# Kernel tuning notes

Hardware: AMD Instinct MI355X
Metric: run time of the kernel (lower is better)

Reference implementation:

```python
import jax, jax.numpy as jnp
import numpy as np

B, T, H, L2 = 131072, 4, 8, 5  # T=4 forced by conv1 in_channels=4; L2 = layers 1..5 of the 6-layer lstm1


def _lstm_dir(xs, w_ih, w_hh, b, h0, c0):
    # xs: [T, B, Din] -> hs: [T, B, H]; PyTorch gate order i, f, g, o
    def step(carry, xt):
        h, c = carry
        g = xt @ w_ih.T + h @ w_hh.T + b
        i, f, gg, o = jnp.split(g, 4, axis=-1)
        c = jax.nn.sigmoid(f) * c + jax.nn.sigmoid(i) * jnp.tanh(gg)
        h = jax.nn.sigmoid(o) * jnp.tanh(c)
        return (h, c), h
    _, hs = jax.lax.scan(step, (h0, c0), xs)
    return hs


def _bilstm(xs, wi_f, wh_f, b_f, wi_b, wh_b, b_b, h0f, c0f, h0b, c0b):
    hf = _lstm_dir(xs, wi_f, wh_f, b_f, h0f, c0f)
    hb = _lstm_dir(xs[::-1], wi_b, wh_b, b_b, h0b, c0b)[::-1]
    return jnp.concatenate([hf, hb], axis=-1)  # [T, B, 2H]


def _conv1d(x, w, b):
    # x: [B, C, L], w: [O, I, K] (torch Conv1d layout)
    y = jax.lax.conv_general_dilated(x, w, (1,), [(0, 0)], dimension_numbers=('NCH', 'OIH', 'NCH'))
    return y + b[None, :, None]


def _deconv1d(x, w, b):
    # torch ConvTranspose1d weight [I, O, K]; stride 1, pad 0 == full conv with flipped kernel
    k = w.shape[-1]
    wk = jnp.flip(jnp.swapaxes(w, 0, 1), -1)  # [O, I, K]
    y = jax.lax.conv_general_dilated(x, wk, (1,), [(k - 1, k - 1)], dimension_numbers=('NCH', 'OIH', 'NCH'))
    return y + b[None, :, None]


def setup_inputs():
    key = jax.random.key(0)
    ks = iter(jax.random.split(key, 32))
    rn = lambda shape, s=0.2: jax.random.normal(next(ks), shape, jnp.float32) * s
    return {
        'x': rn((B, T, 2), 1.0),
        'h0': rn((12, B, H), 1.0),
        'c0': rn((12, B, H), 1.0),
        'w_ih0': rn((2, 4 * H, 2)),
        'w_hh0': rn((2, 4 * H, H)),
        'b_ih0': rn((2, 4 * H)),
        'b_hh0': rn((2, 4 * H)),
        'w_ih': rn((L2, 2, 4 * H, 2 * H)),
        'w_hh': rn((L2, 2, 4 * H, H)),
        'b_ih': rn((L2, 2, 4 * H)),
        'b_hh': rn((L2, 2, 4 * H)),
        'conv1_w': rn((8, 4, 2)), 'conv1_b': rn((8,)),
        'conv2_w': rn((16, 8, 2)), 'conv2_b': rn((16,)),
        'deconv1_w': rn((16, 8, 2)), 'deconv1_b': rn((8,)),
        'deconv2_w': rn((8, 4, 2)), 'deconv2_b': rn((4,)),
        'fc1_w': rn((8, 16)), 'fc1_b': rn((8,)),
        'fc2_w': rn((4, 8)), 'fc2_b': rn((4,)),
    }


def reference(x, h0, c0, w_ih0, w_hh0, b_ih0, b_hh0, w_ih, w_hh, b_ih, b_hh,
              conv1_w, conv1_b, conv2_w, conv2_b, deconv1_w, deconv1_b,
              deconv2_w, deconv2_b, fc1_w, fc1_b, fc2_w, fc2_b):
    xs = jnp.swapaxes(x, 0, 1)  # [T, B, 2]
    y = _bilstm(xs, w_ih0[0], w_hh0[0], b_ih0[0] + b_hh0[0],
                w_ih0[1], w_hh0[1], b_ih0[1] + b_hh0[1],
                h0[0], c0[0], h0[1], c0[1])
    for l in range(L2):  # fixed, small layer count (eval mode: inter-layer dropout off)
        i = 2 * (l + 1)
        y = _bilstm(y, w_ih[l, 0], w_hh[l, 0], b_ih[l, 0] + b_hh[l, 0],
                    w_ih[l, 1], w_hh[l, 1], b_ih[l, 1] + b_hh[l, 1],
                    h0[i], c0[i], h0[i + 1], c0[i + 1])
    y = jax.nn.sigmoid(jnp.swapaxes(y, 0, 1))  # [B, 4, 16]; dim 1 acts as conv channels
    y = _conv1d(y, conv1_w, conv1_b)           # [B, 8, 15]
    y = _conv1d(y, conv2_w, conv2_b)           # [B, 16, 14]
    y = _deconv1d(y, deconv1_w, deconv1_b)     # [B, 8, 15]
    y = _deconv1d(y, deconv2_w, deconv2_b)     # [B, 4, 16]
    y = y @ fc1_w.T + fc1_b                    # [B, 4, 8]
    y = y @ fc2_w.T + fc2_b                    # [B, 4, 4]
    return jnp.tanh(y)
```

## Files before the change

kernel.cpp:

```cpp
#include <hip/hip_runtime.h>
#include <hip/hip_bf16.h>


using f32x2 = __attribute__((ext_vector_type(2))) float;
using f32x4 = __attribute__((ext_vector_type(4))) float;

#define OFF_WIH0 0
#define OFF_WHH0 128
#define OFF_B0   640
#define OFF_WIH  704
#define OFF_WHH  5824
#define OFF_B    8384
#define OFF_M    9024
#define OFF_MB   10048

__device__ __forceinline__ float rcpf_(float x) {
#if __has_builtin(__builtin_amdgcn_rcpf)
    return __builtin_amdgcn_rcpf(x);
#else
    return 1.0f / x;
#endif
}
__device__ __forceinline__ float exp2f_(float x) {
#if __has_builtin(__builtin_amdgcn_exp2f)
    return __builtin_amdgcn_exp2f(x);
#else
    return exp2f(x);
#endif
}
__device__ __forceinline__ float sigm(float x) {
    return rcpf_(1.0f + exp2f_(-1.44269504f * x));
}
__device__ __forceinline__ float tanhx(float x) {
    return fmaf(2.0f, rcpf_(1.0f + exp2f_(-2.88539008f * x)), -1.0f);
}

__global__ __launch_bounds__(256) void prep_all(
    const float* __restrict__ wih0, const float* __restrict__ whh0,
    const float* __restrict__ bih0, const float* __restrict__ bhh0,
    const float* __restrict__ wih,  const float* __restrict__ whh,
    const float* __restrict__ bih,  const float* __restrict__ bhh,
    const float* __restrict__ c1w, const float* __restrict__ c1b,
    const float* __restrict__ c2w, const float* __restrict__ c2b,
    const float* __restrict__ d1w, const float* __restrict__ d1b,
    const float* __restrict__ d2w, const float* __restrict__ d2b,
    const float* __restrict__ f1w, const float* __restrict__ f1b,
    const float* __restrict__ f2w, const float* __restrict__ f2b,
    float* __restrict__ W)
{
    __shared__ float A[13][232];
    __shared__ float Bf[13][232];
    const int tid = threadIdx.x;

    if (blockIdx.x < 36) {
        int t = blockIdx.x * 256 + tid;
        const int n = 36 * 256;
        for (int i = t; i < 128; i += n)  W[OFF_WIH0 + i] = wih0[i];
        for (int i = t; i < 512; i += n)  W[OFF_WHH0 + i] = whh0[i];
        for (int i = t; i < 64; i += n)   W[OFF_B0 + i] = bih0[i] + bhh0[i];
        for (int i = t; i < 5120; i += n) W[OFF_WIH + i] = wih[i];
        for (int i = t; i < 2560; i += n) W[OFF_WHH + i] = whh[i];
        for (int i = t; i < 640; i += n)  W[OFF_B + i] = bih[i] + bhh[i];
        return;
    }
    const int base = (blockIdx.x - 36) * 13;

    for (int idx = tid; idx < 13 * 64; idx += 256) {
        int cl = idx / 64, r = idx % 64;
        A[cl][r] = (base + cl == r) ? 1.0f : 0.0f;
    }
    __syncthreads();
    for (int idx = tid; idx < 13 * 120; idx += 256) {
        int cl = idx / 120, rr = idx % 120; int o = rr / 15, l = rr % 15;
        float acc = (base + cl == 64) ? c1b[o] : 0.0f;
        for (int i = 0; i < 4; i++)
            for (int kk = 0; kk < 2; kk++)
                acc += c1w[(o * 4 + i) * 2 + kk] * A[cl][i * 16 + l + kk];
        Bf[cl][rr] = acc;
    }
    __syncthreads();
    for (int idx = tid; idx < 13 * 224; idx += 256) {
        int cl = idx / 224, rr = idx % 224; int o = rr / 14, l = rr % 14;
        float acc = (base + cl == 64) ? c2b[o] : 0.0f;
        for (int i = 0; i < 8; i++)
            for (int kk = 0; kk < 2; kk++)
                acc += c2w[(o * 8 + i) * 2 + kk] * Bf[cl][i * 15 + l + kk];
        A[cl][rr] = acc;
    }
    __syncthreads();
    for (int idx = tid; idx < 13 * 120; idx += 256) {
        int cl = idx / 120, rr = idx % 120; int o = rr / 15, l = rr % 15;
        float acc = (base + cl == 64) ? d1b[o] : 0.0f;
        for (int i = 0; i < 16; i++)
            for (int kk = 0; kk < 2; kk++) {
                int ls = l - kk;
                if (ls >= 0 && ls < 14)
                    acc += d1w[(i * 8 + o) * 2 + kk] * A[cl][i * 14 + ls];
            }
        Bf[cl][rr] = acc;
    }
    __syncthreads();
    for (int idx = tid; idx < 13 * 64; idx += 256) {
        int cl = idx / 64, rr = idx % 64; int o = rr / 16, l = rr % 16;
        float acc = (base + cl == 64) ? d2b[o] : 0.0f;
        for (int i = 0; i < 8; i++)
            for (int kk = 0; kk < 2; kk++) {
                int ls = l - kk;
                if (ls >= 0 && ls < 15)
                    acc += d2w[(i * 4 + o) * 2 + kk] * Bf[cl][i * 15 + ls];
            }
        A[cl][rr] = acc;
    }
    __syncthreads();
    for (int idx = tid; idx < 13 * 32; idx += 256) {
        int cl = idx / 32, rr = idx % 32; int ch = rr / 8, jj = rr % 8;
        float acc = (base + cl == 64) ? f1b[jj] : 0.0f;
        for (int l = 0; l < 16; l++)
            acc += f1w[jj * 16 + l] * A[cl][ch * 16 + l];
        Bf[cl][rr] = acc;
    }
    __syncthreads();
    for (int idx = tid; idx < 13 * 16; idx += 256) {
        int cl = idx / 16, rr = idx % 16; int ch = rr / 4, m = rr % 4;
        int col = base + cl;
        if (col > 64) continue;
        float acc = (col == 64) ? f2b[m] : 0.0f;
        for (int j = 0; j < 8; j++)
            acc += f2w[m * 8 + j] * Bf[cl][ch * 8 + j];
        if (col < 64) W[OFF_M + rr * 64 + col] = acc;
        else          W[OFF_MB + rr] = acc;
    }
}

template<bool FWD, bool LAST>
__device__ __forceinline__ void layer16(
    const float* __restrict__ Wi, const float* __restrict__ Wh,
    const float* __restrict__ Bs,
    const float* __restrict__ h0s, const float* __restrict__ c0s,
    int gelem0, int u,
    float* const (&lin)[2], float* const (&lout)[2])
{
    f32x4 wiv[4][4];
    f32x4 whv[4][2];
    f32x4 bsv;
#pragma unroll
    for (int g = 0; g < 4; g++) {
        const int r = u + 8 * g;
        const f32x4* wr = reinterpret_cast<const f32x4*>(Wi + r * 16);
        wiv[g][0] = wr[0]; wiv[g][1] = wr[1]; wiv[g][2] = wr[2]; wiv[g][3] = wr[3];
        const f32x4* ur = reinterpret_cast<const f32x4*>(Wh + r * 8);
        whv[g][0] = ur[0]; whv[g][1] = ur[1];
        bsv[g] = Bs[r];
    }
    f32x4 hg[2][2];
    float cc[2];
#pragma unroll
    for (int e = 0; e < 2; e++) {
        const f32x4* hp = reinterpret_cast<const f32x4*>(h0s + (size_t)(gelem0 + e) * 8);
        hg[e][0] = hp[0]; hg[e][1] = hp[1];
        cc[e] = c0s[(size_t)(gelem0 + e) * 8 + u];
    }
    float hreg[2][4];
    const int off = FWD ? 0 : 8;

#pragma unroll
    for (int s = 0; s < 4; s++) {
        const int t = FWD ? s : 3 - s;
        const int tprev = FWD ? t - 1 : t + 1;
        f32x2 acc[2][4];
#pragma unroll
        for (int e = 0; e < 2; e++) {
            const f32x4* ip = reinterpret_cast<const f32x4*>(lin[e] + 16 * t);
            f32x4 i0 = ip[0], i1 = ip[1], i2 = ip[2], i3 = ip[3];
            f32x4 ha, hb;
            if (s == 0) { ha = hg[e][0]; hb = hg[e][1]; }
            else {
                const f32x4* hp = reinterpret_cast<const f32x4*>(lout[e] + 16 * tprev + off);
                ha = hp[0]; hb = hp[1];
            }
            f32x2 xin[8];
            xin[0] = f32x2{i0.x, i0.y}; xin[1] = f32x2{i0.z, i0.w};
            xin[2] = f32x2{i1.x, i1.y}; xin[3] = f32x2{i1.z, i1.w};
            xin[4] = f32x2{i2.x, i2.y}; xin[5] = f32x2{i2.z, i2.w};
            xin[6] = f32x2{i3.x, i3.y}; xin[7] = f32x2{i3.z, i3.w};
            f32x2 hx[4];
            hx[0] = f32x2{ha.x, ha.y}; hx[1] = f32x2{ha.z, ha.w};
            hx[2] = f32x2{hb.x, hb.y}; hx[3] = f32x2{hb.z, hb.w};
#pragma unroll
            for (int g = 0; g < 4; g++) {
                f32x2 a = f32x2{bsv[g], 0.0f};
#pragma unroll
                for (int j = 0; j < 4; j++) {
                    f32x2 wlo = f32x2{wiv[g][j].x, wiv[g][j].y};
                    f32x2 whi = f32x2{wiv[g][j].z, wiv[g][j].w};
                    a = __builtin_elementwise_fma(xin[2 * j], wlo, a);
                    a = __builtin_elementwise_fma(xin[2 * j + 1], whi, a);
                }
#pragma unroll
                for (int j = 0; j < 2; j++) {
                    f32x2 wlo = f32x2{whv[g][j].x, whv[g][j].y};
                    f32x2 whi = f32x2{whv[g][j].z, whv[g][j].w};
                    a = __builtin_elementwise_fma(hx[2 * j], wlo, a);
                    a = __builtin_elementwise_fma(hx[2 * j + 1], whi, a);
                }
                acc[e][g] = a;
            }
        }
#pragma unroll
        for (int e = 0; e < 2; e++) {
            float si = sigm(acc[e][0].x + acc[e][0].y);
            float sf = sigm(acc[e][1].x + acc[e][1].y);
            float tg = tanhx(acc[e][2].x + acc[e][2].y);
            float so = sigm(acc[e][3].x + acc[e][3].y);
            cc[e] = fmaf(sf, cc[e], si * tg);
            float hn = so * tanhx(cc[e]);
            lout[e][16 * t + off + u] = hn;
            if (LAST) hreg[e][s] = hn;
        }
    }
    if (LAST) {
#pragma unroll
        for (int e = 0; e < 2; e++)
#pragma unroll
            for (int s = 0; s < 4; s++) {
                const int t = FWD ? s : 3 - s;
                lout[e][16 * t + off + u] = sigm(hreg[e][s]);
            }
    }
}

template<bool FWD>
__device__ __forceinline__ void layer2(
    const float* __restrict__ Wi, const float* __restrict__ Wh,
    const float* __restrict__ Bs,
    const float* __restrict__ h0s, const float* __restrict__ c0s,
    int gelem0, int u,
    const f32x2 (&xin2)[2][4], float* const (&lout)[2])
{
    f32x2 wiv[4];
    f32x4 whv[4][2];
    f32x4 bsv;
#pragma unroll
    for (int g = 0; g < 4; g++) {
        const int r = u + 8 * g;
        wiv[g] = *reinterpret_cast<const f32x2*>(Wi + r * 2);
        const f32x4* ur = reinterpret_cast<const f32x4*>(Wh + r * 8);
        whv[g][0] = ur[0]; whv[g][1] = ur[1];
        bsv[g] = Bs[r];
    }
    f32x4 hg[2][2];
    float cc[2];
#pragma unroll
    for (int e = 0; e < 2; e++) {
        const f32x4* hp = reinterpret_cast<const f32x4*>(h0s + (size_t)(gelem0 + e) * 8);
        hg[e][0] = hp[0]; hg[e][1] = hp[1];
        cc[e] = c0s[(size_t)(gelem0 + e) * 8 + u];
    }
    const int off = FWD ? 0 : 8;

#pragma unroll
    for (int s = 0; s < 4; s++) {
        const int t = FWD ? s : 3 - s;
        const int tprev = FWD ? t - 1 : t + 1;
        f32x2 acc[2][4];
#pragma unroll
        for (int e = 0; e < 2; e++) {
            f32x4 ha, hb;
            if (s == 0) { ha = hg[e][0]; hb = hg[e][1]; }
            else {
                const f32x4* hp = reinterpret_cast<const f32x4*>(lout[e] + 16 * tprev + off);
                ha = hp[0]; hb = hp[1];
            }
            f32x2 hx[4];
            hx[0] = f32x2{ha.x, ha.y}; hx[1] = f32x2{ha.z, ha.w};
            hx[2] = f32x2{hb.x, hb.y}; hx[3] = f32x2{hb.z, hb.w};
#pragma unroll
            for (int g = 0; g < 4; g++) {
                f32x2 a = __builtin_elementwise_fma(xin2[e][t], wiv[g], f32x2{bsv[g], 0.0f});
#pragma unroll
                for (int j = 0; j < 2; j++) {
                    f32x2 wlo = f32x2{whv[g][j].x, whv[g][j].y};
                    f32x2 whi = f32x2{whv[g][j].z, whv[g][j].w};
                    a = __builtin_elementwise_fma(hx[2 * j], wlo, a);
                    a = __builtin_elementwise_fma(hx[2 * j + 1], whi, a);
                }
                acc[e][g] = a;
            }
        }
#pragma unroll
        for (int e = 0; e < 2; e++) {
            float si = sigm(acc[e][0].x + acc[e][0].y);
            float sf = sigm(acc[e][1].x + acc[e][1].y);
            float tg = tanhx(acc[e][2].x + acc[e][2].y);
            float so = sigm(acc[e][3].x + acc[e][3].y);
            cc[e] = fmaf(sf, cc[e], si * tg);
            lout[e][16 * t + off + u] = so * tanhx(cc[e]);
        }
    }
}

__global__ __launch_bounds__(256, 3) void lstm_main(
    const float* __restrict__ x, const float* __restrict__ h0,
    const float* __restrict__ c0, const float* __restrict__ W,
    float* __restrict__ out, int B)
{
    __shared__ float yb[2][64 * 68];
    const int tid = threadIdx.x;
    const int u = tid & 7;
    const int slot = tid >> 3;
    const int row0 = slot * 2;
    const int gelem0 = blockIdx.x * 64 + row0;

    float* y0[2]; float* y1[2];
#pragma unroll
    for (int e = 0; e < 2; e++) {
        y0[e] = &yb[0][(row0 + e) * 68];
        y1[e] = &yb[1][(row0 + e) * 68];
    }

    f32x2 xin2[2][4];
#pragma unroll
    for (int e = 0; e < 2; e++) {
        const f32x4* xp = reinterpret_cast<const f32x4*>(x + (size_t)(gelem0 + e) * 8);
        f32x4 a = xp[0], b = xp[1];
        xin2[e][0] = f32x2{a.x, a.y}; xin2[e][1] = f32x2{a.z, a.w};
        xin2[e][2] = f32x2{b.x, b.y}; xin2[e][3] = f32x2{b.z, b.w};
    }

    layer2<true>(W + OFF_WIH0, W + OFF_WHH0, W + OFF_B0,
                 h0 + (size_t)0 * B * 8, c0 + (size_t)0 * B * 8,
                 gelem0, u, xin2, y0);
    layer2<false>(W + OFF_WIH0 + 64, W + OFF_WHH0 + 256, W + OFF_B0 + 32,
                  h0 + (size_t)1 * B * 8, c0 + (size_t)1 * B * 8,
                  gelem0, u, xin2, y0);

#pragma unroll
    for (int l = 1; l <= 4; l++) {
        float* const (&lin)[2] = (l & 1) ? y0 : y1;
        float* const (&lout)[2] = (l & 1) ? y1 : y0;
        const float* wi = W + OFF_WIH + (size_t)(l - 1) * 1024;
        const float* wh = W + OFF_WHH + (size_t)(l - 1) * 512;
        const float* bb = W + OFF_B + (size_t)(l - 1) * 64;
        const int si = 2 * l;
        layer16<true, false>(wi, wh, bb,
                             h0 + (size_t)si * B * 8, c0 + (size_t)si * B * 8,
                             gelem0, u, lin, lout);
        layer16<false, false>(wi + 512, wh + 256, bb + 32,
                              h0 + (size_t)(si + 1) * B * 8, c0 + (size_t)(si + 1) * B * 8,
                              gelem0, u, lin, lout);
    }
    {
        const float* wi = W + OFF_WIH + (size_t)4 * 1024;
        const float* wh = W + OFF_WHH + (size_t)4 * 512;
        const float* bb = W + OFF_B + (size_t)4 * 64;
        layer16<true, true>(wi, wh, bb,
                            h0 + (size_t)10 * B * 8, c0 + (size_t)10 * B * 8,
                            gelem0, u, y0, y1);
        layer16<false, true>(wi + 512, wh + 256, bb + 32,
                             h0 + (size_t)11 * B * 8, c0 + (size_t)11 * B * 8,
                             gelem0, u, y0, y1);
    }

    {
        const int o0 = 2 * u, o1 = 2 * u + 1;
        const f32x4* M0 = reinterpret_cast<const f32x4*>(W + OFF_M + o0 * 64);
        const f32x4* M1 = reinterpret_cast<const f32x4*>(W + OFF_M + o1 * 64);
        const float b0 = W[OFF_MB + o0];
        const float b1 = W[OFF_MB + o1];
#pragma unroll
        for (int e = 0; e < 2; e++) {
            float a0 = b0, a1 = b1;
#pragma unroll
            for (int q = 0; q < 16; q++) {
                f32x4 sv = *reinterpret_cast<const f32x4*>(y1[e] + 4 * q);
                f32x4 m0 = M0[q], m1 = M1[q];
                a0 = fmaf(sv.x, m0.x, a0); a0 = fmaf(sv.y, m0.y, a0);
                a0 = fmaf(sv.z, m0.z, a0); a0 = fmaf(sv.w, m0.w, a0);
                a1 = fmaf(sv.x, m1.x, a1); a1 = fmaf(sv.y, m1.y, a1);
                a1 = fmaf(sv.z, m1.z, a1); a1 = fmaf(sv.w, m1.w, a1);
            }
            f32x2 res;
            res.x = tanhx(a0);
            res.y = tanhx(a1);
            *reinterpret_cast<f32x2*>(out + (size_t)(gelem0 + e) * 16 + 2 * u) = res;
        }
    }
}

extern "C" void kernel_launch(void* const* d_in, const int* in_sizes, int n_in,
                              void* d_out, int out_size, void* d_ws, size_t ws_size,
                              hipStream_t stream)
{
    const float* x    = (const float*)d_in[0];
    const float* h0   = (const float*)d_in[1];
    const float* c0   = (const float*)d_in[2];
    const float* wih0 = (const float*)d_in[3];
    const float* whh0 = (const float*)d_in[4];
    const float* bih0 = (const float*)d_in[5];
    const float* bhh0 = (const float*)d_in[6];
    const float* wih  = (const float*)d_in[7];
    const float* whh  = (const float*)d_in[8];
    const float* bih  = (const float*)d_in[9];
    const float* bhh  = (const float*)d_in[10];
    const float* c1w  = (const float*)d_in[11];
    const float* c1b  = (const float*)d_in[12];
    const float* c2w  = (const float*)d_in[13];
    const float* c2b  = (const float*)d_in[14];
    const float* d1w  = (const float*)d_in[15];
    const float* d1b  = (const float*)d_in[16];
    const float* d2w  = (const float*)d_in[17];
    const float* d2b  = (const float*)d_in[18];
    const float* f1w  = (const float*)d_in[19];
    const float* f1b  = (const float*)d_in[20];
    const float* f2w  = (const float*)d_in[21];
    const float* f2b  = (const float*)d_in[22];

    float* W = (float*)d_ws;
    const int B = in_sizes[0] / 8;

    prep_all<<<41, 256, 0, stream>>>(wih0, whh0, bih0, bhh0, wih, whh, bih, bhh,
                                     c1w, c1b, c2w, c2b, d1w, d1b, d2w, d2b,
                                     f1w, f1b, f2w, f2b, W);
    lstm_main<<<B / 64, 256, 0, stream>>>(x, h0, c0, W, (float*)d_out, B);
}
```

Measured before the change: 350.3 us.

## Hoist input projections out of LSTM recurrence and raise occupancy bound

Each LSTM layer now computes the input-to-hidden projections for all four timesteps up front, before the sequential recurrence, so the serial loop only does the small hidden-state matvec plus activations. This shortens the dependent chain per step and lets the input loads and FMAs run without waiting on the previous step. It needs 32 extra live floats per thread for the precomputed gates, while the launch bound minimum blocks per CU goes from 3 to 4, which tightens the register budget and may cause spills.

```diff
diff --git a/kernel.cpp b/kernel.cpp
--- a/kernel.cpp
+++ b/kernel.cpp
@@ -141,51 +141,26 @@
     float* const (&lin)[2], float* const (&lout)[2])
 {
     f32x4 wiv[4][4];
-    f32x4 whv[4][2];
     f32x4 bsv;
 #pragma unroll
     for (int g = 0; g < 4; g++) {
         const int r = u + 8 * g;
         const f32x4* wr = reinterpret_cast<const f32x4*>(Wi + r * 16);
         wiv[g][0] = wr[0]; wiv[g][1] = wr[1]; wiv[g][2] = wr[2]; wiv[g][3] = wr[3];
-        const f32x4* ur = reinterpret_cast<const f32x4*>(Wh + r * 8);
-        whv[g][0] = ur[0]; whv[g][1] = ur[1];
         bsv[g] = Bs[r];
     }
-    f32x4 hg[2][2];
-    float cc[2];
+    float z[2][4][4];
 #pragma unroll
     for (int e = 0; e < 2; e++) {
-        const f32x4* hp = reinterpret_cast<const f32x4*>(h0s + (size_t)(gelem0 + e) * 8);
-        hg[e][0] = hp[0]; hg[e][1] = hp[1];
-        cc[e] = c0s[(size_t)(gelem0 + e) * 8 + u];
-    }
-    float hreg[2][4];
-    const int off = FWD ? 0 : 8;
-
-#pragma unroll
-    for (int s = 0; s < 4; s++) {
-        const int t = FWD ? s : 3 - s;
-        const int tprev = FWD ? t - 1 : t + 1;
-        f32x2 acc[2][4];
-#pragma unroll
-        for (int e = 0; e < 2; e++) {
+#pragma unroll
+        for (int t = 0; t < 4; t++) {
             const f32x4* ip = reinterpret_cast<const f32x4*>(lin[e] + 16 * t);
             f32x4 i0 = ip[0], i1 = ip[1], i2 = ip[2], i3 = ip[3];
-            f32x4 ha, hb;
-            if (s == 0) { ha = hg[e][0]; hb = hg[e][1]; }
-            else {
-                const f32x4* hp = reinterpret_cast<const f32x4*>(lout[e] + 16 * tprev + off);
-                ha = hp[0]; hb = hp[1];
-            }
             f32x2 xin[8];
             xin[0] = f32x2{i0.x, i0.y}; xin[1] = f32x2{i0.z, i0.w};
             xin[2] = f32x2{i1.x, i1.y}; xin[3] = f32x2{i1.z, i1.w};
             xin[4] = f32x2{i2.x, i2.y}; xin[5] = f32x2{i2.z, i2.w};
             xin[6] = f32x2{i3.x, i3.y}; xin[7] = f32x2{i3.z, i3.w};
-            f32x2 hx[4];
-            hx[0] = f32x2{ha.x, ha.y}; hx[1] = f32x2{ha.z, ha.w};
-            hx[2] = f32x2{hb.x, hb.y}; hx[3] = f32x2{hb.z, hb.w};
 #pragma unroll
             for (int g = 0; g < 4; g++) {
                 f32x2 a = f32x2{bsv[g], 0.0f};
@@ -196,22 +171,61 @@
                     a = __builtin_elementwise_fma(xin[2 * j], wlo, a);
                     a = __builtin_elementwise_fma(xin[2 * j + 1], whi, a);
                 }
-#pragma unroll
-                for (int j = 0; j < 2; j++) {
-                    f32x2 wlo = f32x2{whv[g][j].x, whv[g][j].y};
-                    f32x2 whi = f32x2{whv[g][j].z, whv[g][j].w};
-                    a = __builtin_elementwise_fma(hx[2 * j], wlo, a);
-                    a = __builtin_elementwise_fma(hx[2 * j + 1], whi, a);
-                }
-                acc[e][g] = a;
+                z[e][t][g] = a.x + a.y;
             }
         }
+    }
+
+    f32x4 whv[4][2];
+#pragma unroll
+    for (int g = 0; g < 4; g++) {
+        const f32x4* ur = reinterpret_cast<const f32x4*>(Wh + (u + 8 * g) * 8);
+        whv[g][0] = ur[0]; whv[g][1] = ur[1];
+    }
+    f32x4 hg[2][2];
+    float cc[2];
+#pragma unroll
+    for (int e = 0; e < 2; e++) {
+        const f32x4* hp = reinterpret_cast<const f32x4*>(h0s + (size_t)(gelem0 + e) * 8);
+        hg[e][0] = hp[0]; hg[e][1] = hp[1];
+        cc[e] = c0s[(size_t)(gelem0 + e) * 8 + u];
+    }
+    float hreg[2][4];
+    const int off = FWD ? 0 : 8;
+
+#pragma unroll
+    for (int s = 0; s < 4; s++) {
+        const int t = FWD ? s : 3 - s;
+        const int tprev = FWD ? t - 1 : t + 1;
 #pragma unroll
         for (int e = 0; e < 2; e++) {
-            float si = sigm(acc[e][0].x + acc[e][0].y);
-            float sf = sigm(acc[e][1].x + acc[e][1].y);
-            float tg = tanhx(acc[e][2].x + acc[e][2].y);
-            float so = sigm(acc[e][3].x + acc[e][3].y);
+            f32x4 ha, hb;
+            if (s == 0) { ha = hg[e][0]; hb = hg[e][1]; }
+            else {
+                const f32x4* hp = reinterpret_cast<const f32x4*>(lout[e] + 16 * tprev + off);
+                ha = hp[0]; hb = hp[1];
+            }
+            f32x2 hx[4];
+            hx[0] = f32x2{ha.x, ha.y}; hx[1] = f32x2{ha.z, ha.w};
+            hx[2] = f32x2{hb.x, hb.y}; hx[3] = f32x2{hb.z, hb.w};
+            float gate[4];
+#pragma unroll
+            for (int g = 0; g < 4; g++) {
+                f32x2 a = f32x2{z[e][t][g], 0.0f};
+                f32x2 wlo0 = f32x2{whv[g][0].x, whv[g][0].y};
+                f32x2 whi0 = f32x2{whv[g][0].z, whv[g][0].w};
+                f32x2 wlo1 = f32x2{whv[g][1].x, whv[g][1].y};
+                f32x2 whi1 = f32x2{whv[g][1].z, whv[g][1].w};
+                a = __builtin_elementwise_fma(hx[0], wlo0, a);
+                a = __builtin_elementwise_fma(hx[1], whi0, a);
+                a = __builtin_elementwise_fma(hx[2], wlo1, a);
+                a = __builtin_elementwise_fma(hx[3], whi1, a);
+                gate[g] = a.x + a.y;
+            }
+            float si = sigm(gate[0]);
+            float sf = sigm(gate[1]);
+            float tg = tanhx(gate[2]);
+            float so = sigm(gate[3]);
             cc[e] = fmaf(sf, cc[e], si * tg);
             float hn = so * tanhx(cc[e]);
             lout[e][16 * t + off + u] = hn;
@@ -238,15 +252,28 @@
     const f32x2 (&xin2)[2][4], float* const (&lout)[2])
 {
     f32x2 wiv[4];
-    f32x4 whv[4][2];
     f32x4 bsv;
 #pragma unroll
     for (int g = 0; g < 4; g++) {
         const int r = u + 8 * g;
         wiv[g] = *reinterpret_cast<const f32x2*>(Wi + r * 2);
-        const f32x4* ur = reinterpret_cast<const f32x4*>(Wh + r * 8);
+        bsv[g] = Bs[r];
+    }
+    float z[2][4][4];
+#pragma unroll
+    for (int e = 0; e < 2; e++)
+#pragma unroll
+        for (int t = 0; t < 4; t++)
+#pragma unroll
+            for (int g = 0; g < 4; g++)
+                z[e][t][g] = fmaf(xin2[e][t].x, wiv[g].x,
+                             fmaf(xin2[e][t].y, wiv[g].y, bsv[g]));
+
+    f32x4 whv[4][2];
+#pragma unroll
+    for (int g = 0; g < 4; g++) {
+        const f32x4* ur = reinterpret_cast<const f32x4*>(Wh + (u + 8 * g) * 8);
         whv[g][0] = ur[0]; whv[g][1] = ur[1];
-        bsv[g] = Bs[r];
     }
     f32x4 hg[2][2];
     float cc[2];
@@ -262,7 +289,6 @@
     for (int s = 0; s < 4; s++) {
         const int t = FWD ? s : 3 - s;
         const int tprev = FWD ? t - 1 : t + 1;
-        f32x2 acc[2][4];
 #pragma unroll
         for (int e = 0; e < 2; e++) {
             f32x4 ha, hb;
@@ -274,32 +300,31 @@
             f32x2 hx[4];
             hx[0] = f32x2{ha.x, ha.y}; hx[1] = f32x2{ha.z, ha.w};
             hx[2] = f32x2{hb.x, hb.y}; hx[3] = f32x2{hb.z, hb.w};
+            float gate[4];
 #pragma unroll
             for (int g = 0; g < 4; g++) {
-                f32x2 a = __builtin_elementwise_fma(xin2[e][t], wiv[g], f32x2{bsv[g], 0.0f});
-#pragma unroll
-                for (int j = 0; j < 2; j++) {
-                    f32x2 wlo = f32x2{whv[g][j].x, whv[g][j].y};
-                    f32x2 whi = f32x2{whv[g][j].z, whv[g][j].w};
-                    a = __builtin_elementwise_fma(hx[2 * j], wlo, a);
-                    a = __builtin_elementwise_fma(hx[2 * j + 1], whi, a);
-                }
-                acc[e][g] = a;
-            }
-        }
-#pragma unroll
-        for (int e = 0; e < 2; e++) {
-            float si = sigm(acc[e][0].x + acc[e][0].y);
-            float sf = sigm(acc[e][1].x + acc[e][1].y);
-            float tg = tanhx(acc[e][2].x + acc[e][2].y);
-            float so = sigm(acc[e][3].x + acc[e][3].y);
+                f32x2 a = f32x2{z[e][t][g], 0.0f};
+                f32x2 wlo0 = f32x2{whv[g][0].x, whv[g][0].y};
+                f32x2 whi0 = f32x2{whv[g][0].z, whv[g][0].w};
+                f32x2 wlo1 = f32x2{whv[g][1].x, whv[g][1].y};
+                f32x2 whi1 = f32x2{whv[g][1].z, whv[g][1].w};
+                a = __builtin_elementwise_fma(hx[0], wlo0, a);
+                a = __builtin_elementwise_fma(hx[1], whi0, a);
+                a = __builtin_elementwise_fma(hx[2], wlo1, a);
+                a = __builtin_elementwise_fma(hx[3], whi1, a);
+                gate[g] = a.x + a.y;
+            }
+            float si = sigm(gate[0]);
+            float sf = sigm(gate[1]);
+            float tg = tanhx(gate[2]);
+            float so = sigm(gate[3]);
             cc[e] = fmaf(sf, cc[e], si * tg);
             lout[e][16 * t + off + u] = so * tanhx(cc[e]);
         }
     }
 }
 
-__global__ __launch_bounds__(256, 3) void lstm_main(
+__global__ __launch_bounds__(256, 4) void lstm_main(
     const float* __restrict__ x, const float* __restrict__ h0,
     const float* __restrict__ c0, const float* __restrict__ W,
     float* __restrict__ out, int B)
```

Result: slower. 787.7 us (+124.9%).
